# Performance work log

Measured on AMD Instinct MI355X. Metric: run time of the kernel, lower is better.

The kernel has to match this reference:

```python
import jax, jax.numpy as jnp
import numpy as np

# ---- module hyper-parameters (from init_kwargs) ----
K = 31                      # kernel_size
STRIDE = 1
WEIGHT_PRECISION = 4        # -> 3 bit-plane memristor arrays
INPUT_FACTOR = 0.25         # 1/(act_scale*quant_max), frozen after init
OUTPUT_FACTOR = 0.02        # weight_scale*act_scale*quant_max, frozen after init
# DAC/ADC hardware settings
DAC_BITS = 8
DAC_VMAX = 0.6              # hardware input voltage max
ADC_SCALE = 5.0e3           # hardware output current scaling
ADC_PREC_BITS = 8           # quantization step = 2^-8
ADC_RANGE_BITS = 4          # clamp to +/- 2^4
# Synaptogen-style odd read-current polynomials I(v) = c0*v + c1*v^3 + c2*v^5
POLY_HRS = (2.0e-6, 5.0e-8, 1.0e-9)   # high-resistance state
POLY_LRS = (3.0e-4, 4.0e-6, 2.0e-7)   # low-resistance state
# bit weights: plane i (i=0..wp-3) carries 2^(wp-2-i); last plane carries 1
BIT_WEIGHTS = [2.0 ** b for b in range(WEIGHT_PRECISION - 2, 0, -1)] + [1.0]


def _ste_round(x):
    # round with straight-through gradient (quantizer convention)
    return x + jax.lax.stop_gradient(jnp.round(x) - x)


def _dac(x):
    levels = 2 ** (DAC_BITS - 1) - 1
    v = jnp.clip(x, -1.0, 1.0)
    return _ste_round(v * levels) / levels * DAC_VMAX


def _adc(i):
    step = 2.0 ** (-ADC_PREC_BITS)
    lim = 2.0 ** ADC_RANGE_BITS
    return jnp.clip(_ste_round(i * ADC_SCALE / step) * step, -lim, lim)


def _poly_bracket(v2, c):
    # returns (c0 + c1*v^2 + c2*v^4); multiply by v for the odd polynomial
    return c[0] + v2 * (c[1] + v2 * c[2])


def setup_inputs() -> dict:
    key = jax.random.key(0)
    k1, k2, k3, k4 = jax.random.split(key, 4)
    B, F, T = 4, 512, 1000
    return {
        "inputs": jax.random.normal(k1, (B, F, T), jnp.float32),
        "r_pos": jax.random.uniform(k2, (WEIGHT_PRECISION - 1, F, K), jnp.float32),
        "r_neg": jax.random.uniform(k3, (WEIGHT_PRECISION - 1, F, K), jnp.float32),
        "bias": jax.random.normal(k4, (F,), jnp.float32),
    }


def reference(inputs, r_pos, r_neg, bias):
    # inputs: [B, F, T] -> output [B, F, T'] (depthwise memristive conv1d)
    B, F, T = inputs.shape
    v = _dac(inputs * INPUT_FACTOR)
    v = jnp.swapaxes(v, -2, -1)                 # [B, T, F]
    pad = K // 2                                # 'same' padding, zeros mode
    v = jnp.pad(v, ((0, 0), (pad, pad), (0, 0)))
    t_out = (T + 2 * pad - K) // STRIDE + 1
    idx = jnp.arange(t_out)[:, None] * STRIDE + jnp.arange(K)[None, :]
    win = v[:, idx, :]                          # unfold: [B, T', K, F]
    win = jnp.swapaxes(win, 2, 3)               # [B, T', F, K]
    v2 = win * win
    # paired cells: I_pos - I_neg = (r_pos - r_neg) * (I_HRS(v) - I_LRS(v))
    diff = win * (_poly_bracket(v2, POLY_HRS) - _poly_bracket(v2, POLY_LRS))  # [B,T',F,K]
    acc = jnp.zeros((B, t_out, F), inputs.dtype)
    for p in range(WEIGHT_PRECISION - 1):       # small fixed loop over bit planes
        cur = jnp.einsum('btfk,fk->btf', diff, r_pos[p] - r_neg[p])
        acc = acc + _adc(cur) * BIT_WEIGHTS[p]
    out = acc * OUTPUT_FACTOR + bias            # [B, T', F]
    return jnp.swapaxes(out, -2, -1)            # [B, F, T']
```

## Files before the change

### kernel.cpp

```cpp
#include <hip/hip_runtime.h>


#define KW 31
#define PADW 15
#define TT 1000
#define FF 512
#define NP 3
#define BLOCK 256

__global__ __launch_bounds__(BLOCK) void memristor_conv1d_kernel(
    const float* __restrict__ inputs,
    const float* __restrict__ r_pos,
    const float* __restrict__ r_neg,
    const float* __restrict__ bias,
    float* __restrict__ out)
{
    const int bf  = blockIdx.x;
    const int f   = bf & (FF - 1);
    const int tid = threadIdx.x;

    __shared__ float d_lds[TT + 2 * PADW];
    __shared__ float w_lds[NP][KW];

    if (tid < NP * KW) {
        const int p = tid / KW;
        const int k = tid - p * KW;
        const size_t off = ((size_t)p * FF + f) * KW + k;
        w_lds[p][k] = r_pos[off] - r_neg[off];
    }

    const float* in_row = inputs + (size_t)bf * TT;
    for (int t = tid; t < TT + 2 * PADW; t += BLOCK) {
        float dv = 0.0f;
        const int ti = t - PADW;
        if (ti >= 0 && ti < TT) {
            float x = in_row[ti] * 0.25f;
            float v = fminf(fmaxf(x, -1.0f), 1.0f);
            v = rintf(v * 127.0f) / 127.0f * 0.6f;
            const float v2 = v * v;
            const float ph = 2e-06f + v2 * (5e-08f + v2 * 1e-09f);
            const float pl = 3e-04f + v2 * (4e-06f + v2 * 2e-07f);
            dv = v * (ph - pl);
        }
        d_lds[t] = dv;
    }
    __syncthreads();

    const float bv = bias[f];
    float* out_row = out + (size_t)bf * TT;

    for (int t = tid; t < TT; t += BLOCK) {
        float c0 = 0.0f, c1 = 0.0f, c2 = 0.0f;
        #pragma unroll
        for (int k = 0; k < KW; ++k) {
            const float dv = d_lds[t + k];
            c0 = fmaf(dv, w_lds[0][k], c0);
            c1 = fmaf(dv, w_lds[1][k], c1);
            c2 = fmaf(dv, w_lds[2][k], c2);
        }
        float a0 = fminf(fmaxf(rintf(c0 * 1280000.0f) * (1.0f / 256.0f), -16.0f), 16.0f);
        float a1 = fminf(fmaxf(rintf(c1 * 1280000.0f) * (1.0f / 256.0f), -16.0f), 16.0f);
        float a2 = fminf(fmaxf(rintf(c2 * 1280000.0f) * (1.0f / 256.0f), -16.0f), 16.0f);
        out_row[t] = (a0 * 4.0f + a1 * 2.0f + a2) * 0.02f + bv;
    }
}

extern "C" void kernel_launch(void* const* d_in, const int* in_sizes, int n_in,
                              void* d_out, int out_size, void* d_ws, size_t ws_size,
                              hipStream_t stream) {
    const float* inputs = (const float*)d_in[0];
    const float* r_pos  = (const float*)d_in[1];
    const float* r_neg  = (const float*)d_in[2];
    const float* bias   = (const float*)d_in[3];
    float* out = (float*)d_out;

    const int B = in_sizes[0] / (FF * TT);
    dim3 grid(B * FF);
    dim3 block(BLOCK);
    memristor_conv1d_kernel<<<grid, block, 0, stream>>>(inputs, r_pos, r_neg, bias, out);
}
```

Before: 15.46 us.

## Register-tile conv outputs per thread and precompute weight differences in workspace

Each thread now computes 8 consecutive outputs. It loads its input window with float4 loads into registers and applies the DAC and polynomial transform there, so the shared-memory staging and the block barrier are gone. A separate small kernel writes the weight differences into the workspace in an [f][p][k] layout, and the main kernel reads these as broadcast loads. This removes LDS traffic and gives more reuse per thread, but it adds a second kernel launch and leaves 3 of 128 threads idle.

New measurement: 19.99 us. +29.3%, slower.

```diff
diff --git a/kernel.cpp b/kernel.cpp
--- a/kernel.cpp
+++ b/kernel.cpp
@@ -2,67 +2,103 @@
 
 
 #define KW 31
-#define PADW 15
 #define TT 1000
 #define FF 512
 #define NP 3
-#define BLOCK 256
+#define RPT 8
+#define THR 128
+#define NCHUNK 10
 
-__global__ __launch_bounds__(BLOCK) void memristor_conv1d_kernel(
+__device__ __forceinline__ float adc_q(float c) {
+    return fminf(fmaxf(rintf(c * 1280000.0f) * (1.0f / 256.0f), -16.0f), 16.0f);
+}
+
+__global__ void wdiff_kernel(const float* __restrict__ r_pos,
+                             const float* __restrict__ r_neg,
+                             float* __restrict__ wd) {
+    const int i = blockIdx.x * 256 + threadIdx.x;
+    if (i < NP * FF * KW) {
+        const int k  = i % KW;
+        const int pf = i / KW;
+        const int p  = pf / FF;
+        const int f  = pf - p * FF;
+        wd[((size_t)f * NP + p) * KW + k] = r_pos[i] - r_neg[i];
+    }
+}
+
+template <bool USE_WS>
+__global__ __launch_bounds__(THR) void memristor_conv1d_kernel(
     const float* __restrict__ inputs,
+    const float* __restrict__ wdiff,
     const float* __restrict__ r_pos,
     const float* __restrict__ r_neg,
     const float* __restrict__ bias,
     float* __restrict__ out)
 {
-    const int bf  = blockIdx.x;
-    const int f   = bf & (FF - 1);
-    const int tid = threadIdx.x;
+    const int bf = blockIdx.x;
+    const int f  = bf & (FF - 1);
+    const int t  = threadIdx.x;
+    if (t >= TT / RPT) return;
 
-    __shared__ float d_lds[TT + 2 * PADW];
-    __shared__ float w_lds[NP][KW];
+    const float* __restrict__ row = inputs + (size_t)bf * TT;
 
-    if (tid < NP * KW) {
-        const int p = tid / KW;
-        const int k = tid - p * KW;
-        const size_t off = ((size_t)p * FF + f) * KW + k;
-        w_lds[p][k] = r_pos[off] - r_neg[off];
+    float d[NCHUNK * 4];
+    const int c0 = 2 * t - 4;
+    #pragma unroll
+    for (int c = 0; c < NCHUNK; ++c) {
+        const int cc = c0 + c;
+        float4 v = make_float4(0.f, 0.f, 0.f, 0.f);
+        if (cc >= 0 && cc < TT / 4)
+            v = reinterpret_cast<const float4*>(row)[cc];
+        d[4 * c + 0] = v.x; d[4 * c + 1] = v.y; d[4 * c + 2] = v.z; d[4 * c + 3] = v.w;
     }
 
-    const float* in_row = inputs + (size_t)bf * TT;
-    for (int t = tid; t < TT + 2 * PADW; t += BLOCK) {
-        float dv = 0.0f;
-        const int ti = t - PADW;
-        if (ti >= 0 && ti < TT) {
-            float x = in_row[ti] * 0.25f;
-            float v = fminf(fmaxf(x, -1.0f), 1.0f);
-            v = rintf(v * 127.0f) / 127.0f * 0.6f;
-            const float v2 = v * v;
-            const float ph = 2e-06f + v2 * (5e-08f + v2 * 1e-09f);
-            const float pl = 3e-04f + v2 * (4e-06f + v2 * 2e-07f);
-            dv = v * (ph - pl);
+    #pragma unroll
+    for (int i = 1; i <= 38; ++i) {
+        float v = fminf(fmaxf(d[i] * 0.25f, -1.0f), 1.0f);
+        v = rintf(v * 127.0f) * (0.6f / 127.0f);
+        const float v2 = v * v;
+        d[i] = v * fmaf(v2, fmaf(v2, (1e-09f - 2e-07f), (5e-08f - 4e-06f)),
+                        (2e-06f - 3e-04f));
+    }
+
+    float acc[NP][RPT] = {};
+    const float* __restrict__ wf;
+    if (USE_WS) wf = wdiff + (size_t)f * (NP * KW);
+    #pragma unroll
+    for (int k = 0; k < KW; ++k) {
+        float w0, w1, w2;
+        if (USE_WS) {
+            w0 = wf[0 * KW + k]; w1 = wf[1 * KW + k]; w2 = wf[2 * KW + k];
+        } else {
+            const size_t o0 = ((size_t)0 * FF + f) * KW + k;
+            const size_t o1 = ((size_t)1 * FF + f) * KW + k;
+            const size_t o2 = ((size_t)2 * FF + f) * KW + k;
+            w0 = r_pos[o0] - r_neg[o0];
+            w1 = r_pos[o1] - r_neg[o1];
+            w2 = r_pos[o2] - r_neg[o2];
         }
-        d_lds[t] = dv;
+        #pragma unroll
+        for (int r = 0; r < RPT; ++r) {
+            const float dv = d[r + 1 + k];
+            acc[0][r] = fmaf(dv, w0, acc[0][r]);
+            acc[1][r] = fmaf(dv, w1, acc[1][r]);
+            acc[2][r] = fmaf(dv, w2, acc[2][r]);
+        }
     }
-    __syncthreads();
 
     const float bv = bias[f];
-    float* out_row = out + (size_t)bf * TT;
-
-    for (int t = tid; t < TT; t += BLOCK) {
-        float c0 = 0.0f, c1 = 0.0f, c2 = 0.0f;
-        #pragma unroll
-        for (int k = 0; k < KW; ++k) {
-            const float dv = d_lds[t + k];
-            c0 = fmaf(dv, w_lds[0][k], c0);
-            c1 = fmaf(dv, w_lds[1][k], c1);
-            c2 = fmaf(dv, w_lds[2][k], c2);
-        }
-        float a0 = fminf(fmaxf(rintf(c0 * 1280000.0f) * (1.0f / 256.0f), -16.0f), 16.0f);
-        float a1 = fminf(fmaxf(rintf(c1 * 1280000.0f) * (1.0f / 256.0f), -16.0f), 16.0f);
-        float a2 = fminf(fmaxf(rintf(c2 * 1280000.0f) * (1.0f / 256.0f), -16.0f), 16.0f);
-        out_row[t] = (a0 * 4.0f + a1 * 2.0f + a2) * 0.02f + bv;
+    float o[RPT];
+    #pragma unroll
+    for (int r = 0; r < RPT; ++r) {
+        const float a0 = adc_q(acc[0][r]);
+        const float a1 = adc_q(acc[1][r]);
+        const float a2 = adc_q(acc[2][r]);
+        o[r] = fmaf(a0 * 4.0f + a1 * 2.0f + a2, 0.02f, bv);
     }
+    float* __restrict__ orow = out + (size_t)bf * TT + RPT * t;
+    reinterpret_cast<float4*>(orow)[0] = make_float4(o[0], o[1], o[2], o[3]);
+    reinterpret_cast<float4*>(orow)[1] = make_float4(o[4], o[5], o[6], o[7]);
 }
 
 extern "C" void kernel_launch(void* const* d_in, const int* in_sizes, int n_in,
@@ -75,7 +111,18 @@
     float* out = (float*)d_out;
 
     const int B = in_sizes[0] / (FF * TT);
-    dim3 grid(B * FF);
-    dim3 block(BLOCK);
-    memristor_conv1d_kernel<<<grid, block, 0, stream>>>(inputs, r_pos, r_neg, bias, out);
+    const dim3 grid(B * FF);
+    const dim3 block(THR);
+
+    const size_t wd_bytes = (size_t)NP * FF * KW * sizeof(float);
+    if (ws_size >= wd_bytes) {
+        float* wd = (float*)d_ws;
+        wdiff_kernel<<<dim3((NP * FF * KW + 255) / 256), dim3(256), 0, stream>>>(
+            r_pos, r_neg, wd);
+        memristor_conv1d_kernel<true><<<grid, block, 0, stream>>>(
+            inputs, wd, r_pos, r_neg, bias, out);
+    } else {
+        memristor_conv1d_kernel<false><<<grid, block, 0, stream>>>(
+            inputs, nullptr, r_pos, r_neg, bias, out);
+    }
 }
```

## Register-tile 8 outputs per thread with readlane weights and float4 stores

Applied to the files above, without the earlier changes.

Each thread now computes 8 consecutive outputs from a 40-element register window loaded with float4 LDS reads, instead of one output per thread reading LDS for every tap. The 93 weight differences live in lane registers and are broadcast with readlane rather than fetched from LDS. The block shrinks to 128 threads with 125 doing the compute, outputs are written as float4, and the activation polynomial is merged into a single bracket. This cuts LDS traffic and the instruction count per output, at the cost of more registers and fewer active threads per block.

After: 15.76 us. No clear change (+2.0%).

```diff
diff --git a/kernel.cpp b/kernel.cpp
--- a/kernel.cpp
+++ b/kernel.cpp
@@ -6,9 +6,20 @@
 #define TT 1000
 #define FF 512
 #define NP 3
-#define BLOCK 256
+#define RPT 8
+#define THR 128
+#define ACTIVE (TT / RPT)
+#define DL 1032
 
-__global__ __launch_bounds__(BLOCK) void memristor_conv1d_kernel(
+__device__ __forceinline__ float rdlane_f(float v, int lane) {
+    return __int_as_float(__builtin_amdgcn_readlane(__float_as_int(v), lane));
+}
+
+__device__ __forceinline__ float adc_q(float c) {
+    return fminf(fmaxf(rintf(c * 1280000.0f) * (1.0f / 256.0f), -16.0f), 16.0f);
+}
+
+__global__ __launch_bounds__(THR) void memristor_kernel(
     const float* __restrict__ inputs,
     const float* __restrict__ r_pos,
     const float* __restrict__ r_neg,
@@ -19,50 +30,74 @@
     const int f   = bf & (FF - 1);
     const int tid = threadIdx.x;
 
-    __shared__ float d_lds[TT + 2 * PADW];
-    __shared__ float w_lds[NP][KW];
+    __shared__ float d_lds[DL];
 
-    if (tid < NP * KW) {
-        const int p = tid / KW;
-        const int k = tid - p * KW;
-        const size_t off = ((size_t)p * FF + f) * KW + k;
-        w_lds[p][k] = r_pos[off] - r_neg[off];
+    const int lane = tid & 63;
+    float w_lo = 0.0f, w_hi = 0.0f;
+    if (lane < NP * KW) {
+        const int p = lane / KW, k = lane - p * KW;
+        const size_t o = ((size_t)p * FF + f) * KW + k;
+        w_lo = r_pos[o] - r_neg[o];
+    }
+    if (lane + 64 < NP * KW) {
+        const int l2 = lane + 64;
+        const int p = l2 / KW, k = l2 - p * KW;
+        const size_t o = ((size_t)p * FF + f) * KW + k;
+        w_hi = r_pos[o] - r_neg[o];
     }
 
-    const float* in_row = inputs + (size_t)bf * TT;
-    for (int t = tid; t < TT + 2 * PADW; t += BLOCK) {
+    const float* __restrict__ row = inputs + (size_t)bf * TT;
+    for (int i = tid; i < DL; i += THR) {
         float dv = 0.0f;
-        const int ti = t - PADW;
+        const int ti = i - PADW;
         if (ti >= 0 && ti < TT) {
-            float x = in_row[ti] * 0.25f;
-            float v = fminf(fmaxf(x, -1.0f), 1.0f);
-            v = rintf(v * 127.0f) / 127.0f * 0.6f;
+            float v = fminf(fmaxf(row[ti] * 0.25f, -1.0f), 1.0f);
+            v = rintf(v * 127.0f) * (0.6f / 127.0f);
             const float v2 = v * v;
-            const float ph = 2e-06f + v2 * (5e-08f + v2 * 1e-09f);
-            const float pl = 3e-04f + v2 * (4e-06f + v2 * 2e-07f);
-            dv = v * (ph - pl);
+            dv = v * fmaf(v2, fmaf(v2, (1e-09f - 2e-07f), (5e-08f - 4e-06f)),
+                          (2e-06f - 3e-04f));
         }
-        d_lds[t] = dv;
+        d_lds[i] = dv;
     }
     __syncthreads();
 
+    if (tid >= ACTIVE) return;
+
+    const int t8 = tid * RPT;
+    float win[40];
+    {
+        const float4* dl4 = reinterpret_cast<const float4*>(&d_lds[t8]);
+        #pragma unroll
+        for (int c = 0; c < 10; ++c) {
+            const float4 v = dl4[c];
+            win[4 * c + 0] = v.x; win[4 * c + 1] = v.y;
+            win[4 * c + 2] = v.z; win[4 * c + 3] = v.w;
+        }
+    }
+
+    float acc[NP][RPT] = {};
+    #pragma unroll
+    for (int k = 0; k < KW; ++k) {
+        #pragma unroll
+        for (int p = 0; p < NP; ++p) {
+            const int flat = p * KW + k;
+            const float w = rdlane_f(flat < 64 ? w_lo : w_hi, flat & 63);
+            #pragma unroll
+            for (int r = 0; r < RPT; ++r)
+                acc[p][r] = fmaf(win[r + k], w, acc[p][r]);
+        }
+    }
+
     const float bv = bias[f];
-    float* out_row = out + (size_t)bf * TT;
-
-    for (int t = tid; t < TT; t += BLOCK) {
-        float c0 = 0.0f, c1 = 0.0f, c2 = 0.0f;
-        #pragma unroll
-        for (int k = 0; k < KW; ++k) {
-            const float dv = d_lds[t + k];
-            c0 = fmaf(dv, w_lds[0][k], c0);
-            c1 = fmaf(dv, w_lds[1][k], c1);
-            c2 = fmaf(dv, w_lds[2][k], c2);
-        }
-        float a0 = fminf(fmaxf(rintf(c0 * 1280000.0f) * (1.0f / 256.0f), -16.0f), 16.0f);
-        float a1 = fminf(fmaxf(rintf(c1 * 1280000.0f) * (1.0f / 256.0f), -16.0f), 16.0f);
-        float a2 = fminf(fmaxf(rintf(c2 * 1280000.0f) * (1.0f / 256.0f), -16.0f), 16.0f);
-        out_row[t] = (a0 * 4.0f + a1 * 2.0f + a2) * 0.02f + bv;
+    float o[RPT];
+    #pragma unroll
+    for (int r = 0; r < RPT; ++r) {
+        o[r] = fmaf(adc_q(acc[0][r]) * 4.0f + adc_q(acc[1][r]) * 2.0f + adc_q(acc[2][r]),
+                    0.02f, bv);
     }
+    float* __restrict__ orow = out + (size_t)bf * TT + t8;
+    reinterpret_cast<float4*>(orow)[0] = make_float4(o[0], o[1], o[2], o[3]);
+    reinterpret_cast<float4*>(orow)[1] = make_float4(o[4], o[5], o[6], o[7]);
 }
 
 extern "C" void kernel_launch(void* const* d_in, const int* in_sizes, int n_in,
@@ -75,7 +110,6 @@
     float* out = (float*)d_out;
 
     const int B = in_sizes[0] / (FF * TT);
-    dim3 grid(B * FF);
-    dim3 block(BLOCK);
-    memristor_conv1d_kernel<<<grid, block, 0, stream>>>(inputs, r_pos, r_neg, bias, out);
+    memristor_kernel<<<dim3(B * FF), dim3(THR), 0, stream>>>(
+        inputs, r_pos, r_neg, bias, out);
 }
```
